# Performance work log

Measured on AMD Instinct MI355X. Metric: run time of the kernel, lower is better.

## Reference

```python
import jax, jax.numpy as jnp
import numpy as np

N_EMBD = 256; N_HEAD = 16; CTX = 2048
V_HD = 32; KV_RANK = 32; Q_RANK = 96
ROPE_HD = 64; NOPE_HD = 32; HEAD_D = ROPE_HD + NOPE_HD  # 96
N_KEEP = CTX // 4  # 512
C_CURV = 1.0
EPS = 1e-6
B, T = 2, 2048


def rmsnorm(x, w):
    return x * jax.lax.rsqrt(jnp.mean(x * x, axis=-1, keepdims=True) + EPS) * w


def logmap(x, u, c):
    # log map from hyperbolic point x toward u (Poincare ball, curvature c)
    xn = jnp.linalg.norm(x, axis=-1, keepdims=True)
    sf = 2.0 / (1.0 + c * xn ** 2)                      # scaling_factor(x, c)
    mx = -x
    un = jnp.linalg.norm(u, axis=-1, keepdims=True)
    ip = jnp.sum(mx * u, axis=-1, keepdims=True)
    num = (1 + 2 * c * ip + c * un ** 2) * mx + (1 - c * xn ** 2) * u
    den = 1 + 2 * c * ip + (c ** 2) * (xn ** 2) * (un ** 2)
    mob = num / den                                      # mobius_addition(-x, u, c)
    an = jnp.linalg.norm(mob, axis=-1, keepdims=True)
    cf = 2.0 / (sf * (c ** 0.5))
    arg = jnp.clip(jnp.sqrt(c) * jnp.sqrt(an), -0.999, 0.999)
    return cf * jnp.arctanh(arg) * (mob / an)


def rope_apply(x, cos_seq, sin_seq):
    # x: [B,H,T,D]; cos/sin: [T,D//2] -> broadcast [1,1,T,D//2]
    c = cos_seq[None, None]; s = sin_seq[None, None]
    xr, xi = jnp.split(x, 2, axis=-1)
    return jnp.concatenate([xr * c - xi * s, xr * s + xi * c], axis=-1)


def attn(q, k, v, causal):
    d = q.shape[-1]
    s = jnp.einsum('bhqd,bhkd->bhqk', q, k) / jnp.sqrt(jnp.asarray(d, q.dtype))
    if causal:
        mask = jnp.tril(jnp.ones((s.shape[-2], s.shape[-1]), bool))
        s = jnp.where(mask, s, -jnp.inf)
    p = jax.nn.softmax(s, axis=-1)
    return jnp.einsum('bhqk,bhkd->bhqd', p, v)


def setup_inputs() -> dict:
    key = jax.random.key(0)
    ks = jax.random.split(key, 20)
    w = lambda k, shp: (jax.random.normal(k, shp, jnp.float32) * 0.02)
    NOPE_DIM = N_HEAD * NOPE_HD   # 512
    ROPE_DIM = N_HEAD * ROPE_HD   # 1024
    VAL_DIM = N_HEAD * V_HD       # 512
    # precompute_freqs_cis(rope_head_dim, ctx_len)
    freqs = 1.0 / (10000.0 ** (np.arange(0, ROPE_HD, 2, dtype=np.float32) / ROPE_HD))
    t = np.arange(CTX, dtype=np.float32)
    ang = np.outer(t, freqs)
    return {
        'x': jax.random.normal(ks[0], (B, T, N_EMBD), jnp.float32),
        'W_cq': w(ks[1], (N_EMBD, Q_RANK)),
        'q_norm_w': jnp.ones((Q_RANK,), jnp.float32),
        'W_dqn': w(ks[2], (Q_RANK, NOPE_DIM)),
        'W_dqr': w(ks[3], (Q_RANK, ROPE_DIM)),
        'W_ckv': w(ks[4], (N_EMBD, KV_RANK)),
        'kv_norm_w': jnp.ones((KV_RANK,), jnp.float32),
        'W_dkn': w(ks[5], (KV_RANK, NOPE_DIM)),
        'W_dv': w(ks[6], (KV_RANK, VAL_DIM)),
        'W_kr': w(ks[7], (N_EMBD, ROPE_HD)),
        'W_imp': w(ks[8], (N_EMBD, 1)),
        'b_imp': jnp.zeros((1,), jnp.float32),
        'W_selk': w(ks[9], (N_EMBD, N_HEAD * HEAD_D)),
        'W_selv': w(ks[10], (N_EMBD, VAL_DIM)),
        'W_wink': w(ks[11], (N_EMBD, N_HEAD * HEAD_D)),
        'W_winv': w(ks[12], (N_EMBD, VAL_DIM)),
        'W_gate': w(ks[13], (N_EMBD, 3)),
        'b_gate': jnp.zeros((3,), jnp.float32),
        'W_proj': w(ks[14], (N_HEAD * V_HD, N_EMBD)),
        'cos_f': jnp.asarray(np.cos(ang)),
        'sin_f': jnp.asarray(np.sin(ang)),
    }


def reference(x, W_cq, q_norm_w, W_dqn, W_dqr, W_ckv, kv_norm_w, W_dkn, W_dv, W_kr,
              W_imp, b_imp, W_selk, W_selv, W_wink, W_winv, W_gate, b_gate, W_proj,
              cos_f, sin_f):
    Bx, Tx, C = x.shape
    ref = jnp.pad(x[:, :-1, :], ((0, 0), (1, 0), (0, 0)))   # calculate_reference_point
    xh = logmap(ref, x, C_CURV)
    # compressed query path
    nq = rmsnorm(xh @ W_cq, q_norm_w)
    qn = (nq @ W_dqn).reshape(Bx, Tx, N_HEAD, NOPE_HD).transpose(0, 2, 1, 3)
    qr = (nq @ W_dqr).reshape(Bx, Tx, N_HEAD, ROPE_HD).transpose(0, 2, 1, 3)
    qr = rope_apply(qr, cos_f[:Tx], sin_f[:Tx])
    q = jnp.concatenate([qn, qr], axis=-1)                  # [B,H,T,96]
    # branch gate
    bw = jax.nn.softmax(jnp.mean(x @ W_gate + b_gate, axis=1), axis=-1)  # [B,3]
    # compressed KV path
    nkv = rmsnorm(x @ W_ckv, kv_norm_w)
    kn = (nkv @ W_dkn).reshape(Bx, Tx, N_HEAD, NOPE_HD).transpose(0, 2, 1, 3)
    v = (nkv @ W_dv).reshape(Bx, Tx, N_HEAD, V_HD).transpose(0, 2, 1, 3)
    kr = rope_apply((x @ W_kr)[:, None], cos_f[:Tx], sin_f[:Tx])  # [B,1,T,64]
    kr = jnp.broadcast_to(kr, (Bx, N_HEAD, Tx, ROPE_HD))
    k = jnp.concatenate([kn, kr], axis=-1)
    out_cmp = attn(q, k, v, causal=True)
    # token-selection branch (top-k important tokens, sorted)
    scores = (x @ W_imp + b_imp)[..., 0]                    # [B,T]
    _, idx = jax.lax.top_k(scores, min(N_KEEP, Tx))
    idx = jnp.sort(idx, axis=1)
    sel = jnp.take_along_axis(x, idx[:, :, None], axis=1)   # [B,K,C]
    sk = (sel @ W_selk).reshape(Bx, -1, N_HEAD, HEAD_D).transpose(0, 2, 1, 3)
    sv = (sel @ W_selv).reshape(Bx, -1, N_HEAD, V_HD).transpose(0, 2, 1, 3)
    out_sel = attn(q, sk, sv, causal=False)
    # sliding-window branch (training path -> full sequence, causal)
    wk = (x @ W_wink).reshape(Bx, Tx, N_HEAD, HEAD_D).transpose(0, 2, 1, 3)
    wv = (x @ W_winv).reshape(Bx, Tx, N_HEAD, V_HD).transpose(0, 2, 1, 3)
    out_win = attn(q, wk, wv, causal=True)
    w3 = bw[:, :, None, None, None]
    out = w3[:, 0] * out_cmp + w3[:, 1] * out_sel + w3[:, 2] * out_win
    out = out.transpose(0, 2, 1, 3).reshape(Bx, Tx, N_HEAD * V_HD)
    return out @ W_proj
```

## Files before the change

kernel.cpp:

```cpp
#include <hip/hip_runtime.h>
#include <hip/hip_bf16.h>
#include <math.h>

#define TT 2048
#define NE 256
#define NHEAD 16

typedef __attribute__((ext_vector_type(8))) short bf16x8;
typedef __attribute__((ext_vector_type(4))) float f32x4;
typedef __attribute__((ext_vector_type(16))) float f32x16;
typedef unsigned short ushort;
typedef __attribute__((ext_vector_type(8))) unsigned short us8;

__device__ __forceinline__ short f2bf(float x) {
  __hip_bfloat16 h = __float2bfloat16(x);
  return *reinterpret_cast<short*>(&h);
}
__device__ __forceinline__ float bf2f(ushort u) {
  unsigned v = ((unsigned)u) << 16;
  return __uint_as_float(v);
}

__global__ __launch_bounds__(256) void prep_kernel(
    const float* __restrict__ x, ushort* __restrict__ xhb, ushort* __restrict__ xbf,
    const float* __restrict__ W_dqn, const float* __restrict__ W_dqr,
    const float* __restrict__ W_dkn, const float* __restrict__ W_dv,
    const float* __restrict__ W_selk, const float* __restrict__ W_selv,
    const float* __restrict__ W_wink, const float* __restrict__ W_winv,
    const float* __restrict__ W_proj, const float* __restrict__ W_cq,
    const float* __restrict__ W_ckv, const float* __restrict__ W_kr,
    const float* __restrict__ W_gate, const float* __restrict__ W_imp,
    ushort* __restrict__ Wt_q, ushort* __restrict__ Wt_kv,
    ushort* __restrict__ Wt_sel, ushort* __restrict__ Wt_win,
    ushort* __restrict__ Wt_proj, ushort* __restrict__ Wt_cq,
    ushort* __restrict__ Wt_nkv, float* __restrict__ gacc) {
  __shared__ float red[16];
  int bx = blockIdx.x, tid = threadIdx.x;
  if (bx < 4096) {
    int row = bx;
    int t = row & (TT - 1);
    float uv = x[row * NE + tid];
    float rv = (t == 0) ? 0.f : x[row * NE - NE + tid];
    xbf[row * NE + tid] = (ushort)f2bf(uv);
    float a = rv * rv, bq = uv * uv, c2 = -rv * uv;
#pragma unroll
    for (int off = 32; off > 0; off >>= 1) {
      a += __shfl_down(a, off, 64);
      bq += __shfl_down(bq, off, 64);
      c2 += __shfl_down(c2, off, 64);
    }
    if ((tid & 63) == 0) {
      int w = tid >> 6;
      red[w] = a; red[4 + w] = bq; red[8 + w] = c2;
    }
    __syncthreads();
    float xn2 = red[0] + red[1] + red[2] + red[3];
    float un2 = red[4] + red[5] + red[6] + red[7];
    float ip  = red[8] + red[9] + red[10] + red[11];
    float den = 1.f + 2.f * ip + xn2 * un2;
    float mob = ((1.f + 2.f * ip + un2) * (-rv) + (1.f - xn2) * uv) / den;
    float m2 = mob * mob;
#pragma unroll
    for (int off = 32; off > 0; off >>= 1) m2 += __shfl_down(m2, off, 64);
    if ((tid & 63) == 0) red[12 + (tid >> 6)] = m2;
    __syncthreads();
    float an2 = red[12] + red[13] + red[14] + red[15];
    float an = sqrtf(an2);
    float cf = 1.f + xn2;
    float arg = fminf(sqrtf(an), 0.999f);
    xhb[row * NE + tid] = (ushort)f2bf(cf * atanhf(arg) * mob / an);
    return;
  }
  int i = (bx - 4096) * 256 + tid;
  const float scale = 0.147244458176154f;
  if (i < 147456) {
    int k = i / 1536, n = i - k * 1536;
    float v = (n < 512) ? W_dqn[(size_t)k * 512 + n] : W_dqr[(size_t)k * 1024 + (n - 512)];
    Wt_q[(size_t)n * 96 + k] = (ushort)f2bf(v * scale);
  } else if (i < 180224) {
    int j = i - 147456;
    int k = j >> 10, n = j & 1023;
    float v = (n < 512) ? W_dkn[(size_t)k * 512 + n] : W_dv[(size_t)k * 512 + (n - 512)];
    Wt_kv[(size_t)n * 32 + k] = (ushort)f2bf(v);
  } else if (i < 704512) {
    int j = i - 180224;
    int k = j >> 11, n = j & 2047;
    float v = (n < 1536) ? W_selk[(size_t)k * 1536 + n] : W_selv[(size_t)k * 512 + (n - 1536)];
    Wt_sel[(size_t)n * 256 + k] = (ushort)f2bf(v);
  } else if (i < 1228800) {
    int j = i - 704512;
    int k = j >> 11, n = j & 2047;
    float v = (n < 1536) ? W_wink[(size_t)k * 1536 + n] : W_winv[(size_t)k * 512 + (n - 1536)];
    Wt_win[(size_t)n * 256 + k] = (ushort)f2bf(v);
  } else if (i < 1359872) {
    int j = i - 1228800;
    int k = j >> 8, n = j & 255;
    Wt_proj[(size_t)n * 512 + k] = (ushort)f2bf(W_proj[(size_t)k * 256 + n]);
  } else if (i < 1392640) {
    int j = i - 1359872;
    int k = j >> 7, n = j & 127;
    float v = (n < 96) ? W_cq[(size_t)k * 96 + n] : 0.f;
    Wt_cq[(size_t)n * 256 + k] = (ushort)f2bf(v);
  } else if (i < 1425408) {
    int j = i - 1392640;
    int k = j >> 7, n = j & 127;
    float v;
    if (n < 32) v = W_ckv[(size_t)k * 32 + n];
    else if (n < 96) v = W_kr[(size_t)k * 64 + (n - 32)];
    else if (n < 99) v = W_gate[(size_t)k * 3 + (n - 96)];
    else if (n == 99) v = W_imp[k];
    else v = 0.f;
    Wt_nkv[(size_t)n * 256 + k] = (ushort)f2bf(v);
  } else if (i < 1425414) {
    gacc[i - 1425408] = 0.f;
  }
}

__global__ __launch_bounds__(256) void gemm_kernel(const ushort* __restrict__ A,
                                                   const ushort* __restrict__ Bt,
                                                   void* __restrict__ Out,
                                                   const ushort* __restrict__ A2,
                                                   const ushort* __restrict__ Bt2,
                                                   void* __restrict__ Out2,
                                                   const int* __restrict__ selidx2,
                                                   const float* __restrict__ cosp,
                                                   const float* __restrict__ sinp,
                                                   float* __restrict__ gateacc,
                                                   int K, int ldo, int obf16, int ropemode,
                                                   int K2, int ldo2, int obf2, int rope2,
                                                   int xlim2, int ylim2) {
  __shared__ __align__(16) short As[128 * 40];
  __shared__ __align__(16) short Bs[128 * 40];
  const int* selidx = nullptr;
  if (blockIdx.z == 1) {
    if ((int)blockIdx.x >= xlim2 || (int)blockIdx.y >= ylim2) return;
    A = A2; Bt = Bt2; Out = Out2; selidx = selidx2;
    K = K2; ldo = ldo2; obf16 = obf2; ropemode = rope2;
  }
  int m0 = blockIdx.x * 128, n0 = blockIdx.y * 128;
  int tid = threadIdx.x;
  int wv = tid >> 6, lane = tid & 63;
  int l15 = lane & 15, quad = lane >> 4;
  int wm = wv >> 1, wn = wv & 1;

  int r = tid >> 1, seg = tid & 1;
  int arow = m0 + r;
  if (selidx) arow = ((arow >> 9) * TT) + selidx[m0 + r];
  const ushort* ga = A + (size_t)arow * K + seg * 16;
  const ushort* gb = Bt + (size_t)(n0 + r) * K + seg * 16;

  f32x4 acc[4][4];
#pragma unroll
  for (int i = 0; i < 4; ++i)
#pragma unroll
    for (int j = 0; j < 4; ++j) acc[i][j] = (f32x4){0.f, 0.f, 0.f, 0.f};

  int nk = K >> 5;
  us8 apre0 = *(const us8*)ga, apre1 = *(const us8*)(ga + 8);
  us8 bpre0 = *(const us8*)gb, bpre1 = *(const us8*)(gb + 8);
  for (int kk = 0; kk < nk; ++kk) {
    __syncthreads();
    *(us8*)(As + r * 40 + seg * 16) = apre0;
    *(us8*)(As + r * 40 + seg * 16 + 8) = apre1;
    *(us8*)(Bs + r * 40 + seg * 16) = bpre0;
    *(us8*)(Bs + r * 40 + seg * 16 + 8) = bpre1;
    __syncthreads();
    if (kk + 1 < nk) {
      apre0 = *(const us8*)(ga + (kk + 1) * 32);
      apre1 = *(const us8*)(ga + (kk + 1) * 32 + 8);
      bpre0 = *(const us8*)(gb + (kk + 1) * 32);
      bpre1 = *(const us8*)(gb + (kk + 1) * 32 + 8);
    }
    bf16x8 af[4], bf[4];
#pragma unroll
    for (int mf = 0; mf < 4; ++mf)
      af[mf] = *(const bf16x8*)(As + (wm * 64 + mf * 16 + l15) * 40 + quad * 8);
#pragma unroll
    for (int nf = 0; nf < 4; ++nf)
      bf[nf] = *(const bf16x8*)(Bs + (wn * 64 + nf * 16 + l15) * 40 + quad * 8);
#pragma unroll
    for (int mf = 0; mf < 4; ++mf)
#pragma unroll
      for (int nf = 0; nf < 4; ++nf)
        acc[mf][nf] = __builtin_amdgcn_mfma_f32_16x16x32_bf16(af[mf], bf[nf], acc[mf][nf], 0, 0, 0);
  }

  if (ropemode && blockIdx.y >= 4) {
#pragma unroll
    for (int mf = 0; mf < 4; ++mf) {
#pragma unroll
      for (int nf = 0; nf < 2; ++nf) {
        int dd = nf * 16 + l15;
#pragma unroll
        for (int reg = 0; reg < 4; ++reg) {
          int row = m0 + wm * 64 + mf * 16 + quad * 4 + reg;
          int t = row & (TT - 1);
          float c = cosp[t * 32 + dd], s = sinp[t * 32 + dd];
          float xr = acc[mf][nf][reg], xi = acc[mf][nf + 2][reg];
          int col = n0 + wn * 64 + nf * 16 + l15;
          size_t oi = (size_t)row * ldo + col;
          ((ushort*)Out)[oi] = (ushort)f2bf(xr * c - xi * s);
          ((ushort*)Out)[oi + 32] = (ushort)f2bf(xr * s + xi * c);
        }
      }
    }
    return;
  }
#pragma unroll
  for (int mf = 0; mf < 4; ++mf) {
#pragma unroll
    for (int nf = 0; nf < 4; ++nf) {
#pragma unroll
      for (int reg = 0; reg < 4; ++reg) {
        int row = m0 + wm * 64 + mf * 16 + quad * 4 + reg;
        int col = n0 + wn * 64 + nf * 16 + l15;
        size_t oi = (size_t)row * ldo + col;
        float v = acc[mf][nf][reg];
        if (obf16) ((ushort*)Out)[oi] = (ushort)f2bf(v);
        else ((float*)Out)[oi] = v;
      }
    }
  }
  if (gateacc != nullptr && blockIdx.z == 1 && wn == 1 && l15 < 3) {
    float ssum = 0.f;
#pragma unroll
    for (int mf = 0; mf < 4; ++mf)
#pragma unroll
      for (int reg = 0; reg < 4; ++reg) ssum += acc[mf][2][reg];
    atomicAdd(&gateacc[(m0 >> 11) * 3 + l15], ssum);
  }
}

__global__ __launch_bounds__(128) void norm_kernel(const float* __restrict__ nkvraw,
                                                   const float* __restrict__ nqraw,
                                                   const float* __restrict__ x,
                                                   const float* __restrict__ W_imp,
                                                   const float* __restrict__ b_imp,
                                                   const float* __restrict__ kvnw,
                                                   const float* __restrict__ qnw,
                                                   const float* __restrict__ cos_t,
                                                   const float* __restrict__ sin_t,
                                                   ushort* __restrict__ nkvb,
                                                   ushort* __restrict__ krbf,
                                                   float* __restrict__ scores,
                                                   ushort* __restrict__ nqb) {
  int tid = threadIdx.x;
  if (blockIdx.x < 4096) {
    int row = blockIdx.x;
    int t = row & (TT - 1);
    if (tid < 32) {
      float v = nkvraw[(size_t)row * 128 + tid];
      float ss = v * v;
#pragma unroll
      for (int off = 16; off > 0; off >>= 1) ss += __shfl_xor(ss, off, 32);
      nkvb[(size_t)row * 32 + tid] = (ushort)f2bf(v * rsqrtf(ss / 32.f + 1e-6f) * kvnw[tid]);
    } else if (tid < 64) {
      int dd = tid - 32;
      float xr = nkvraw[(size_t)row * 128 + 32 + dd];
      float xi = nkvraw[(size_t)row * 128 + 64 + dd];
      float c = cos_t[t * 32 + dd], s = sin_t[t * 32 + dd];
      krbf[(size_t)row * 64 + dd] = (ushort)f2bf(xr * c - xi * s);
      krbf[(size_t)row * 64 + dd + 32] = (ushort)f2bf(xr * s + xi * c);
    } else {
      int lane = tid - 64;
      float p = 0.f;
#pragma unroll
      for (int k = 0; k < 4; ++k) p += x[(size_t)row * 256 + lane + k * 64] * W_imp[lane + k * 64];
#pragma unroll
      for (int off = 32; off > 0; off >>= 1) p += __shfl_down(p, off, 64);
      if (lane == 0) scores[row] = p + b_imp[0];
    }
  } else {
    int row = blockIdx.x - 4096;
    __shared__ float red2[2];
    float v = (tid < 96) ? nqraw[(size_t)row * 128 + tid] : 0.f;
    float p = v * v;
#pragma unroll
    for (int off = 32; off > 0; off >>= 1) p += __shfl_down(p, off, 64);
    if ((tid & 63) == 0) red2[tid >> 6] = p;
    __syncthreads();
    float ss = red2[0] + red2[1];
    float sc = rsqrtf(ss / 96.f + 1e-6f);
    if (tid < 96) nqb[(size_t)row * 96 + tid] = (ushort)f2bf(v * sc * qnw[tid]);
  }
}

__global__ __launch_bounds__(1024) void topk_rank_kernel(const float* __restrict__ scores,
                                                         int* __restrict__ flags) {
  int b = blockIdx.y, blk = blockIdx.x;
  int tid = threadIdx.x;
  __shared__ unsigned sk[TT];
#pragma unroll
  for (int e = 0; e < 2; ++e) {
    int i = tid + e * 1024;
    float s = scores[b * TT + i];
    unsigned u = __float_as_uint(s);
    u = (u & 0x80000000u) ? ~u : (u | 0x80000000u);
    sk[i] = u;
  }
  __syncthreads();
  int e = blk * 64 + (tid >> 4);
  int sub = tid & 15;
  unsigned u = sk[e];
  int r = 0;
  int j0 = sub * 128;
#pragma unroll 8
  for (int j = j0; j < j0 + 128; ++j) {
    unsigned v = sk[j];
    r += (int)((v > u) || (v == u && j < e));
  }
#pragma unroll
  for (int off = 8; off > 0; off >>= 1) r += __shfl_down(r, off, 16);
  if (sub == 0) flags[b * TT + e] = (r < 512) ? 1 : 0;
}

__global__ __launch_bounds__(1024) void topk_scan_kernel(const int* __restrict__ flags,
                                                         int* __restrict__ selidx) {
  int b = blockIdx.x, tid = threadIdx.x;
  __shared__ int wsum[16];
  int2 f = *(const int2*)(flags + b * TT + 2 * tid);
  int local = f.x + f.y;
  int lane = tid & 63, wv = tid >> 6;
  int sc = local;
#pragma unroll
  for (int off = 1; off < 64; off <<= 1) {
    int t = __shfl_up(sc, off, 64);
    if (lane >= off) sc += t;
  }
  if (lane == 63) wsum[wv] = sc;
  __syncthreads();
  int woff = 0;
  for (int w = 0; w < wv; ++w) woff += wsum[w];
  int p0 = woff + (sc - local) + f.x;
  int p1 = p0 + f.y;
  if (f.x) selidx[b * 512 + p0 - 1] = 2 * tid;
  if (f.y) selidx[b * 512 + p1 - 1] = 2 * tid + 1;
}

__global__ __launch_bounds__(512, 4) void flash_fused_kernel(
    const ushort* __restrict__ qbf,
    const ushort* __restrict__ kv,
    const ushort* __restrict__ krbf,
    const ushort* __restrict__ selt,
    const ushort* __restrict__ wint,
    const float* __restrict__ gacc,
    const float* __restrict__ b_gate,
    ushort* __restrict__ attout) {
  __shared__ __align__(16) short smem[13312 + 13312 + 4608 + 256];
  short* Qsm = smem;
  short* Ksm = smem + 13312;
  short* Vtm = smem + 26624;
  float* Ls  = (float*)(smem + 31232);

  int bx = blockIdx.x;
  int j = bx >> 5;
  int qtile = (j < 8) ? (15 - 2 * j) : (2 * (j - 8));
  int bh = bx & 31;
  int b = bh >> 4, h = bh & 15;
  int tid = threadIdx.x;
  int wv = tid >> 6;
  int qsub = wv >> 1;
  int khalf = wv & 1;
  int lane = tid & 63;
  int l31 = lane & 31, half = lane >> 5;

  float w0, w1, w2;
  {
    float g0 = gacc[b * 3 + 0] * (1.0f / 2048.0f) + b_gate[0];
    float g1 = gacc[b * 3 + 1] * (1.0f / 2048.0f) + b_gate[1];
    float g2 = gacc[b * 3 + 2] * (1.0f / 2048.0f) + b_gate[2];
    float mx = fmaxf(g0, fmaxf(g1, g2));
    float e0 = expf(g0 - mx), e1 = expf(g1 - mx), e2 = expf(g2 - mx);
    float inv = 1.f / (e0 + e1 + e2);
    w0 = e0 * inv; w1 = e1 * inv; w2 = e2 * inv;
  }

  int qrow0 = qtile * 128;
  for (int i = tid; i < 128 * 24; i += 512) {
    int qi = i / 24, dp = (i - qi * 24) * 4;
    int col = (dp < 32) ? (h * 32 + dp) : (512 + h * 64 + (dp - 32));
    *(ushort4*)(Qsm + qi * 104 + dp) =
        *(const ushort4*)(qbf + (size_t)(b * TT + qrow0 + qi) * 1536 + col);
  }

  short* kdst[3];
#pragma unroll
  for (int c = 0; c < 3; ++c) {
    int i = c * 512 + tid;
    int kj = i / 24, dp = (i - kj * 24) * 4;
    kdst[c] = &Ksm[kj * 104 + dp];
  }
  int vd0 = (tid & 15) * 2, vkjp = (tid >> 4) * 2;
  short* vdsta = &Vtm[(vd0 + 0) * 72 + vkjp];
  short* vdstb = &Vtm[(vd0 + 1) * 72 + vkjp];

  f32x16 oacc;
#pragma unroll
  for (int r2 = 0; r2 < 16; ++r2) oacc[r2] = 0.f;

#define PREFETCH(KP, VA, VB)                                  \
  {                                                           \
    _Pragma("unroll") for (int c = 0; c < 3; ++c) {           \
      KP[c] = *(const ushort4*)ksrc[c];                       \
      ksrc[c] += kstep[c];                                    \
    }                                                         \
    VA = *(const ushort2*)vsrcA;                              \
    VB = *(const ushort2*)vsrcB;                              \
    vsrcA += vstep;                                           \
    vsrcB += vstep;                                           \
  }

#define COMMIT(KP, VA, VB, SL)                                           \
  {                                                                      \
    _Pragma("unroll") for (int c = 0; c < 3; ++c)                        \
      *(ushort4*)(kdst[c] + (SL) * (64 * 104)) = KP[c];                  \
    *(unsigned*)(vdsta + (SL) * (32 * 72)) =                             \
        (unsigned)VA.x | ((unsigned)VB.x << 16);                         \
    *(unsigned*)(vdstb + (SL) * (32 * 72)) =                             \
        (unsigned)VA.y | ((unsigned)VB.y << 16);                         \
  }

  for (int s = 0; s < 3; ++s) {
    const ushort *kb1, *kb2, *vb;
    size_t krs1, krs2, vrs;
    int split, Tk, causal;
    if (s == 0) {
      kb1 = kv + h * 32;        krs1 = 1024; split = 32;
      kb2 = krbf;               krs2 = 64;
      vb = kv + 512 + h * 32;   vrs = 1024;
      Tk = TT; causal = 1;
    } else if (s == 1) {
      kb1 = selt + h * 96;      krs1 = 2048; split = 96;
      kb2 = selt;               krs2 = 2048;
      vb = selt + 1536 + h * 32; vrs = 2048;
      Tk = 512; causal = 0;
    } else {
      kb1 = wint + h * 96;      krs1 = 2048; split = 96;
      kb2 = wint;               krs2 = 2048;
      vb = wint + 1536 + h * 32; vrs = 2048;
      Tk = TT; causal = 1;
    }
    size_t bTk = (size_t)b * Tk;

    const ushort* ksrc[3];
    int kstep[3];
#pragma unroll
    for (int c = 0; c < 3; ++c) {
      int i = c * 512 + tid;
      int kj = i / 24, dp = (i - kj * 24) * 4;
      if (dp < split) { ksrc[c] = kb1 + (bTk + kj) * krs1 + dp; kstep[c] = (int)(64 * krs1); }
      else            { ksrc[c] = kb2 + (bTk + kj) * krs2 + (dp - split); kstep[c] = (int)(64 * krs2); }
    }
    const ushort* vsrcA = vb + (bTk + vkjp) * vrs + vd0;
    const ushort* vsrcB = vb + (bTk + vkjp + 1) * vrs + vd0;
    int vstep = (int)(64 * vrs);

    ushort4 kpre0[3], kpre1[3];
    ushort2 vpa0, vpb0, vpa1, vpb1;

    f32x16 of;
#pragma unroll
    for (int r2 = 0; r2 < 16; ++r2) of[r2] = 0.f;
    float lsum = 0.f;

    auto do_tile = [&](int kt, const short* Kss, const short* Vss) {
      int krow0 = kt * 64;
      const short* Qrow = Qsm + (qsub * 32 + l31) * 104 + half * 8;
      f32x16 sfT[2];
#pragma unroll
      for (int r2 = 0; r2 < 16; ++r2) { sfT[0][r2] = 0.f; sfT[1][r2] = 0.f; }
#pragma unroll
      for (int ks = 0; ks < 6; ++ks) {
        bf16x8 qk = *(const bf16x8*)(Qrow + ks * 16);
#pragma unroll
        for (int kb = 0; kb < 2; ++kb) {
          bf16x8 ak = *(const bf16x8*)(Kss + (kb * 32 + l31) * 104 + ks * 16 + half * 8);
          sfT[kb] = __builtin_amdgcn_mfma_f32_32x32x16_bf16(ak, qk, sfT[kb], 0, 0, 0);
        }
      }
      int qg = qrow0 + qsub * 32 + l31;
      int domask = causal && (kt >= 2 * qtile);
      unsigned w01[2][4], w23[2][4];
#pragma unroll
      for (int kb = 0; kb < 2; ++kb) {
#pragma unroll
        for (int gg = 0; gg < 4; ++gg) {
          int key0 = krow0 + kb * 32 + 8 * gg + 4 * half;
          float t0 = sfT[kb][gg * 4 + 0];
          float t1 = sfT[kb][gg * 4 + 1];
          float t2 = sfT[kb][gg * 4 + 2];
          float t3 = sfT[kb][gg * 4 + 3];
          if (domask) {
            if (key0 + 0 > qg) t0 = -INFINITY;
            if (key0 + 1 > qg) t1 = -INFINITY;
            if (key0 + 2 > qg) t2 = -INFINITY;
            if (key0 + 3 > qg) t3 = -INFINITY;
          }
          float p0 = __builtin_amdgcn_exp2f(fminf(t0, 43.3f));
          float p1 = __builtin_amdgcn_exp2f(fminf(t1, 43.3f));
          float p2 = __builtin_amdgcn_exp2f(fminf(t2, 43.3f));
          float p3 = __builtin_amdgcn_exp2f(fminf(t3, 43.3f));
          lsum += (p0 + p1) + (p2 + p3);
          asm("v_cvt_pk_bf16_f32 %0, %1, %2" : "=v"(w01[kb][gg]) : "v"(p0), "v"(p1));
          asm("v_cvt_pk_bf16_f32 %0, %1, %2" : "=v"(w23[kb][gg]) : "v"(p2), "v"(p3));
        }
      }
#pragma unroll
      for (int ks2 = 0; ks2 < 4; ++ks2) {
        int kb = ks2 >> 1, gA = 2 * (ks2 & 1);
        unsigned a0 = w01[kb][gA], b0 = w01[kb][gA + 1];
        unsigned a1 = w23[kb][gA], b1 = w23[kb][gA + 1];
        asm("v_permlane32_swap_b32 %0, %1" : "+v"(a0), "+v"(b0));
        asm("v_permlane32_swap_b32 %0, %1" : "+v"(a1), "+v"(b1));
        union { unsigned u[4]; bf16x8 v; } ap;
        ap.u[0] = a0; ap.u[1] = a1; ap.u[2] = b0; ap.u[3] = b1;
        bf16x8 bv = *(const bf16x8*)(Vss + l31 * 72 + ks2 * 16 + half * 8);
        of = __builtin_amdgcn_mfma_f32_32x32x16_bf16(ap.v, bv, of, 0, 0, 0);
      }
    };

    int nkt = causal ? (2 * qtile + 2) : 8;
    PREFETCH(kpre0, vpa0, vpb0);
    PREFETCH(kpre1, vpa1, vpb1);
    for (int kt = 0; kt < nkt; kt += 2) {
      __syncthreads();
      COMMIT(kpre0, vpa0, vpb0, 0);
      COMMIT(kpre1, vpa1, vpb1, 1);
      if (kt + 2 < nkt) PREFETCH(kpre0, vpa0, vpb0);
      if (kt + 3 < nkt) PREFETCH(kpre1, vpa1, vpb1);
      __syncthreads();
      if (khalf == 0) do_tile(kt, Ksm, Vtm);
      else            do_tile(kt + 1, Ksm + 64 * 104, Vtm + 32 * 72);
    }

    lsum += __shfl_xor(lsum, 32, 64);
    __syncthreads();
    float* red = (float*)Ksm;
    int rbase = (qsub * 64 + lane) * 17;
    if (khalf == 1) {
#pragma unroll
      for (int r2 = 0; r2 < 16; ++r2) red[rbase + r2] = of[r2];
      red[rbase + 16] = lsum;
    }
    __syncthreads();
    if (khalf == 0) {
#pragma unroll
      for (int r2 = 0; r2 < 16; ++r2) of[r2] += red[rbase + r2];
      lsum += red[rbase + 16];
      if (half == 0) Ls[qsub * 32 + l31] = lsum;
    }
    asm volatile("s_waitcnt lgkmcnt(0)" ::: "memory");
    if (khalf == 0) {
      float wgt = (s == 0) ? w0 : ((s == 1) ? w1 : w2);
#pragma unroll
      for (int reg = 0; reg < 16; ++reg) {
        int ql = (reg & 3) + 8 * (reg >> 2) + 4 * half;
        oacc[reg] += of[reg] * (wgt / Ls[qsub * 32 + ql]);
      }
    }
  }
#undef PREFETCH
#undef COMMIT

  if (khalf == 0) {
#pragma unroll
    for (int reg = 0; reg < 16; ++reg) {
      int trow = qrow0 + qsub * 32 + (reg & 3) + 8 * (reg >> 2) + 4 * half;
      attout[(size_t)(b * TT + trow) * 512 + h * 32 + l31] = (ushort)f2bf(oacc[reg]);
    }
  }
}

extern "C" void kernel_launch(void* const* d_in, const int* in_sizes, int n_in,
                              void* d_out, int out_size, void* d_ws, size_t ws_size,
                              hipStream_t stream) {
  const float* x      = (const float*)d_in[0];
  const float* W_cq   = (const float*)d_in[1];
  const float* qnw    = (const float*)d_in[2];
  const float* W_dqn  = (const float*)d_in[3];
  const float* W_dqr  = (const float*)d_in[4];
  const float* W_ckv  = (const float*)d_in[5];
  const float* kvnw   = (const float*)d_in[6];
  const float* W_dkn  = (const float*)d_in[7];
  const float* W_dv   = (const float*)d_in[8];
  const float* W_kr   = (const float*)d_in[9];
  const float* W_imp  = (const float*)d_in[10];
  const float* b_imp  = (const float*)d_in[11];
  const float* W_selk = (const float*)d_in[12];
  const float* W_selv = (const float*)d_in[13];
  const float* W_wink = (const float*)d_in[14];
  const float* W_winv = (const float*)d_in[15];
  const float* W_gate = (const float*)d_in[16];
  const float* b_gate = (const float*)d_in[17];
  const float* W_proj = (const float*)d_in[18];
  const float* cos_f  = (const float*)d_in[19];
  const float* sin_f  = (const float*)d_in[20];
  float* out = (float*)d_out;
  float* ws  = (float*)d_ws;

  size_t off = 0;
  auto alloc = [&](size_t n) {
    float* p = ws + off;
    off += (n + 255) & ~(size_t)255;
    return p;
  };
  const int ROWS = 2 * TT;
  ushort* xbf     = (ushort*)alloc((size_t)ROWS * 128);
  ushort* xhb     = (ushort*)alloc((size_t)ROWS * 128);
  float* nqraw    = alloc((size_t)ROWS * 128);
  float* nkvraw   = alloc((size_t)ROWS * 128);
  ushort* nqb     = (ushort*)alloc((size_t)ROWS * 48);
  ushort* qbf     = (ushort*)alloc((size_t)ROWS * 768);
  ushort* nkvb    = (ushort*)alloc((size_t)ROWS * 16);
  ushort* kvtmp   = (ushort*)alloc((size_t)ROWS * 512);
  ushort* krbf    = (ushort*)alloc((size_t)ROWS * 32);
  float* scores   = alloc(ROWS);
  float* gacc     = alloc(8);
  int* selidx     = (int*)alloc(1024);
  int* selflags   = (int*)alloc(ROWS);
  ushort* seltmp  = (ushort*)alloc((size_t)1024 * 1024);
  ushort* wintmp  = (ushort*)alloc((size_t)ROWS * 1024);
  ushort* attoutb = (ushort*)alloc((size_t)ROWS * 256);
  ushort* Wt_q    = (ushort*)alloc((size_t)1536 * 48);
  ushort* Wt_kv   = (ushort*)alloc((size_t)1024 * 16);
  ushort* Wt_sel  = (ushort*)alloc((size_t)2048 * 128);
  ushort* Wt_win  = (ushort*)alloc((size_t)2048 * 128);
  ushort* Wt_proj = (ushort*)alloc((size_t)256 * 256);
  ushort* Wt_cq   = (ushort*)alloc((size_t)128 * 128);
  ushort* Wt_nkv  = (ushort*)alloc((size_t)128 * 128);

  prep_kernel<<<4096 + 5569, 256, 0, stream>>>(
      x, xhb, xbf,
      W_dqn, W_dqr, W_dkn, W_dv, W_selk, W_selv, W_wink, W_winv, W_proj,
      W_cq, W_ckv, W_kr, W_gate, W_imp,
      Wt_q, Wt_kv, Wt_sel, Wt_win, Wt_proj, Wt_cq, Wt_nkv, gacc);

  gemm_kernel<<<dim3(32, 1, 2), 256, 0, stream>>>(
      xhb, Wt_cq, nqraw, xbf, Wt_nkv, nkvraw,
      nullptr, nullptr, nullptr, gacc,
      256, 128, 0, 0, 256, 128, 0, 0, 32, 1);

  norm_kernel<<<2 * ROWS, 128, 0, stream>>>(nkvraw, nqraw, x, W_imp, b_imp, kvnw, qnw,
                                            cos_f, sin_f, nkvb, krbf, scores, nqb);

  gemm_kernel<<<dim3(32, 12, 2), 256, 0, stream>>>(
      nqb, Wt_q, qbf, nkvb, Wt_kv, kvtmp,
      nullptr, cos_f, sin_f, nullptr,
      96, 1536, 1, 1, 32, 1024, 1, 0, 32, 8);

  topk_rank_kernel<<<dim3(32, 2), 1024, 0, stream>>>(scores, selflags);
  topk_scan_kernel<<<2, 1024, 0, stream>>>(selflags, selidx);

  gemm_kernel<<<dim3(32, 16, 2), 256, 0, stream>>>(
      xbf, Wt_win, wintmp, xbf, Wt_sel, seltmp,
      selidx, nullptr, nullptr, nullptr,
      256, 2048, 1, 0, 256, 2048, 1, 0, 8, 16);

  flash_fused_kernel<<<512, 512, 0, stream>>>(qbf, kvtmp, krbf, seltmp, wintmp,
                                              gacc, b_gate, attoutb);

  gemm_kernel<<<dim3(32, 2, 1), 256, 0, stream>>>(
      attoutb, Wt_proj, out, nullptr, nullptr, nullptr,
      nullptr, nullptr, nullptr, nullptr,
      512, 256, 0, 0, 0, 0, 0, 0, 0, 0);
}
```

Baseline: 276.8 us.

## Fuse RMSNorm, key RoPE and importance scores into first GEMM epilogue

Removes the separate norm_kernel by doing the q/kv RMSNorm, the rope on the key-rope projection, the importance score and the gate accumulation inside the epilogue of the first low-rank GEMM. Row sums of squares are reduced with shuffles across the tile and through shared memory, which is reused from the A/B tiles. This avoids writing and rereading the fp32 raw projection buffers and saves one kernel launch. In exchange the GEMM epilogue gains extra syncs and branching, and its stores are scattered.

New measurement: 274.4 us. Within noise of the previous version (-0.8%).

```diff
diff --git a/kernel.cpp b/kernel.cpp
--- a/kernel.cpp
+++ b/kernel.cpp
@@ -126,11 +126,18 @@
                                                    const float* __restrict__ cosp,
                                                    const float* __restrict__ sinp,
                                                    float* __restrict__ gateacc,
+                                                   const float* __restrict__ kvnw,
+                                                   const float* __restrict__ qnw,
+                                                   const float* __restrict__ bimp,
+                                                   ushort* __restrict__ krbf_o,
+                                                   float* __restrict__ scores_o,
+                                                   int fusenorm,
                                                    int K, int ldo, int obf16, int ropemode,
                                                    int K2, int ldo2, int obf2, int rope2,
                                                    int xlim2, int ylim2) {
-  __shared__ __align__(16) short As[128 * 40];
-  __shared__ __align__(16) short Bs[128 * 40];
+  __shared__ __align__(16) short gsm[2 * 128 * 40];
+  short* As = gsm;
+  short* Bs = gsm + 128 * 40;
   const int* selidx = nullptr;
   if (blockIdx.z == 1) {
     if ((int)blockIdx.x >= xlim2 || (int)blockIdx.y >= ylim2) return;
@@ -185,6 +192,119 @@
         acc[mf][nf] = __builtin_amdgcn_mfma_f32_16x16x32_bf16(af[mf], bf[nf], acc[mf][nf], 0, 0, 0);
   }
 
+  if (fusenorm) {
+    __syncthreads();
+    float* sc = (float*)gsm;
+    if (blockIdx.z == 0) {
+      float ss[4][4];
+#pragma unroll
+      for (int mf = 0; mf < 4; ++mf)
+#pragma unroll
+        for (int reg = 0; reg < 4; ++reg) {
+          float p = acc[mf][0][reg] * acc[mf][0][reg] + acc[mf][1][reg] * acc[mf][1][reg];
+          if (wn == 0) p += acc[mf][2][reg] * acc[mf][2][reg] + acc[mf][3][reg] * acc[mf][3][reg];
+#pragma unroll
+          for (int off = 8; off > 0; off >>= 1) p += __shfl_xor(p, off, 64);
+          ss[mf][reg] = p;
+        }
+      if (l15 == 0) {
+#pragma unroll
+        for (int mf = 0; mf < 4; ++mf)
+#pragma unroll
+          for (int reg = 0; reg < 4; ++reg)
+            sc[wn * 128 + wm * 64 + mf * 16 + quad * 4 + reg] = ss[mf][reg];
+      }
+      __syncthreads();
+#pragma unroll
+      for (int mf = 0; mf < 4; ++mf) {
+#pragma unroll
+        for (int nf = 0; nf < 4; ++nf) {
+          if (wn == 1 && nf >= 2) continue;
+          int col = wn * 64 + nf * 16 + l15;
+#pragma unroll
+          for (int reg = 0; reg < 4; ++reg) {
+            int rl = wm * 64 + mf * 16 + quad * 4 + reg;
+            float sstot = sc[rl] + sc[128 + rl];
+            float sca = rsqrtf(sstot / 96.f + 1e-6f) * qnw[col];
+            ((ushort*)Out)[(size_t)(m0 + rl) * 96 + col] = (ushort)f2bf(acc[mf][nf][reg] * sca);
+          }
+        }
+      }
+    } else {
+      if (wn == 1 && l15 < 3) {
+        float g = 0.f;
+#pragma unroll
+        for (int mf = 0; mf < 4; ++mf)
+#pragma unroll
+          for (int reg = 0; reg < 4; ++reg) g += acc[mf][2][reg];
+        atomicAdd(&gateacc[(m0 >> 11) * 3 + l15], g);
+      }
+      if (wn == 1 && l15 == 3) {
+#pragma unroll
+        for (int mf = 0; mf < 4; ++mf)
+#pragma unroll
+          for (int reg = 0; reg < 4; ++reg)
+            scores_o[m0 + wm * 64 + mf * 16 + quad * 4 + reg] = acc[mf][2][reg] + bimp[0];
+      }
+      if (wn == 0) {
+#pragma unroll
+        for (int mf = 0; mf < 4; ++mf) {
+          float ssr[4];
+#pragma unroll
+          for (int reg = 0; reg < 4; ++reg) {
+            float p = acc[mf][0][reg] * acc[mf][0][reg] + acc[mf][1][reg] * acc[mf][1][reg];
+#pragma unroll
+            for (int off = 8; off > 0; off >>= 1) p += __shfl_xor(p, off, 64);
+            ssr[reg] = p;
+          }
+#pragma unroll
+          for (int nf = 0; nf < 2; ++nf) {
+            int col = nf * 16 + l15;
+#pragma unroll
+            for (int reg = 0; reg < 4; ++reg) {
+              int rl = wm * 64 + mf * 16 + quad * 4 + reg;
+              float sca = rsqrtf(ssr[reg] / 32.f + 1e-6f) * kvnw[col];
+              ((ushort*)Out)[(size_t)(m0 + rl) * 32 + col] = (ushort)f2bf(acc[mf][nf][reg] * sca);
+            }
+          }
+        }
+      }
+      if (wn == 1) {
+#pragma unroll
+        for (int mf = 0; mf < 4; ++mf)
+#pragma unroll
+          for (int nf = 0; nf < 2; ++nf) {
+            int dd = nf * 16 + l15;
+#pragma unroll
+            for (int reg = 0; reg < 4; ++reg) {
+              int rl = wm * 64 + mf * 16 + quad * 4 + reg;
+              sc[rl * 33 + dd] = acc[mf][nf][reg];
+            }
+          }
+      }
+      __syncthreads();
+      if (wn == 0) {
+#pragma unroll
+        for (int mf = 0; mf < 4; ++mf)
+#pragma unroll
+          for (int nf = 2; nf < 4; ++nf) {
+            int dd = (nf - 2) * 16 + l15;
+#pragma unroll
+            for (int reg = 0; reg < 4; ++reg) {
+              int rl = wm * 64 + mf * 16 + quad * 4 + reg;
+              int grow = m0 + rl;
+              int t = grow & (TT - 1);
+              float c = cosp[t * 32 + dd], s = sinp[t * 32 + dd];
+              float xr = acc[mf][nf][reg], xi = sc[rl * 33 + dd];
+              krbf_o[(size_t)grow * 64 + dd] = (ushort)f2bf(xr * c - xi * s);
+              krbf_o[(size_t)grow * 64 + dd + 32] = (ushort)f2bf(xr * s + xi * c);
+            }
+          }
+      }
+    }
+    return;
+  }
+
   if (ropemode && blockIdx.y >= 4) {
 #pragma unroll
     for (int mf = 0; mf < 4; ++mf) {
@@ -220,68 +340,6 @@
         else ((float*)Out)[oi] = v;
       }
     }
-  }
-  if (gateacc != nullptr && blockIdx.z == 1 && wn == 1 && l15 < 3) {
-    float ssum = 0.f;
-#pragma unroll
-    for (int mf = 0; mf < 4; ++mf)
-#pragma unroll
-      for (int reg = 0; reg < 4; ++reg) ssum += acc[mf][2][reg];
-    atomicAdd(&gateacc[(m0 >> 11) * 3 + l15], ssum);
-  }
-}
-
-__global__ __launch_bounds__(128) void norm_kernel(const float* __restrict__ nkvraw,
-                                                   const float* __restrict__ nqraw,
-                                                   const float* __restrict__ x,
-                                                   const float* __restrict__ W_imp,
-                                                   const float* __restrict__ b_imp,
-                                                   const float* __restrict__ kvnw,
-                                                   const float* __restrict__ qnw,
-                                                   const float* __restrict__ cos_t,
-                                                   const float* __restrict__ sin_t,
-                                                   ushort* __restrict__ nkvb,
-                                                   ushort* __restrict__ krbf,
-                                                   float* __restrict__ scores,
-                                                   ushort* __restrict__ nqb) {
-  int tid = threadIdx.x;
-  if (blockIdx.x < 4096) {
-    int row = blockIdx.x;
-    int t = row & (TT - 1);
-    if (tid < 32) {
-      float v = nkvraw[(size_t)row * 128 + tid];
-      float ss = v * v;
-#pragma unroll
-      for (int off = 16; off > 0; off >>= 1) ss += __shfl_xor(ss, off, 32);
-      nkvb[(size_t)row * 32 + tid] = (ushort)f2bf(v * rsqrtf(ss / 32.f + 1e-6f) * kvnw[tid]);
-    } else if (tid < 64) {
-      int dd = tid - 32;
-      float xr = nkvraw[(size_t)row * 128 + 32 + dd];
-      float xi = nkvraw[(size_t)row * 128 + 64 + dd];
-      float c = cos_t[t * 32 + dd], s = sin_t[t * 32 + dd];
-      krbf[(size_t)row * 64 + dd] = (ushort)f2bf(xr * c - xi * s);
-      krbf[(size_t)row * 64 + dd + 32] = (ushort)f2bf(xr * s + xi * c);
-    } else {
-      int lane = tid - 64;
-      float p = 0.f;
-#pragma unroll
-      for (int k = 0; k < 4; ++k) p += x[(size_t)row * 256 + lane + k * 64] * W_imp[lane + k * 64];
-#pragma unroll
-      for (int off = 32; off > 0; off >>= 1) p += __shfl_down(p, off, 64);
-      if (lane == 0) scores[row] = p + b_imp[0];
-    }
-  } else {
-    int row = blockIdx.x - 4096;
-    __shared__ float red2[2];
-    float v = (tid < 96) ? nqraw[(size_t)row * 128 + tid] : 0.f;
-    float p = v * v;
-#pragma unroll
-    for (int off = 32; off > 0; off >>= 1) p += __shfl_down(p, off, 64);
-    if ((tid & 63) == 0) red2[tid >> 6] = p;
-    __syncthreads();
-    float ss = red2[0] + red2[1];
-    float sc = rsqrtf(ss / 96.f + 1e-6f);
-    if (tid < 96) nqb[(size_t)row * 96 + tid] = (ushort)f2bf(v * sc * qnw[tid]);
   }
 }
 
@@ -607,8 +665,6 @@
   const int ROWS = 2 * TT;
   ushort* xbf     = (ushort*)alloc((size_t)ROWS * 128);
   ushort* xhb     = (ushort*)alloc((size_t)ROWS * 128);
-  float* nqraw    = alloc((size_t)ROWS * 128);
-  float* nkvraw   = alloc((size_t)ROWS * 128);
   ushort* nqb     = (ushort*)alloc((size_t)ROWS * 48);
   ushort* qbf     = (ushort*)alloc((size_t)ROWS * 768);
   ushort* nkvb    = (ushort*)alloc((size_t)ROWS * 16);
@@ -636,16 +692,15 @@
       Wt_q, Wt_kv, Wt_sel, Wt_win, Wt_proj, Wt_cq, Wt_nkv, gacc);
 
   gemm_kernel<<<dim3(32, 1, 2), 256, 0, stream>>>(
-      xhb, Wt_cq, nqraw, xbf, Wt_nkv, nkvraw,
-      nullptr, nullptr, nullptr, gacc,
-      256, 128, 0, 0, 256, 128, 0, 0, 32, 1);
-
-  norm_kernel<<<2 * ROWS, 128, 0, stream>>>(nkvraw, nqraw, x, W_imp, b_imp, kvnw, qnw,
-                                            cos_f, sin_f, nkvb, krbf, scores, nqb);
+      xhb, Wt_cq, nqb, xbf, Wt_nkv, nkvb,
+      nullptr, cos_f, sin_f, gacc,
+      kvnw, qnw, b_imp, krbf, scores, 1,
+      256, 96, 1, 0, 256, 32, 1, 0, 32, 1);
 
   gemm_kernel<<<dim3(32, 12, 2), 256, 0, stream>>>(
       nqb, Wt_q, qbf, nkvb, Wt_kv, kvtmp,
       nullptr, cos_f, sin_f, nullptr,
+      nullptr, nullptr, nullptr, nullptr, nullptr, 0,
       96, 1536, 1, 1, 32, 1024, 1, 0, 32, 8);
 
   topk_rank_kernel<<<dim3(32, 2), 1024, 0, stream>>>(scores, selflags);
@@ -654,6 +709,7 @@
   gemm_kernel<<<dim3(32, 16, 2), 256, 0, stream>>>(
       xbf, Wt_win, wintmp, xbf, Wt_sel, seltmp,
       selidx, nullptr, nullptr, nullptr,
+      nullptr, nullptr, nullptr, nullptr, nullptr, 0,
       256, 2048, 1, 0, 256, 2048, 1, 0, 8, 16);
 
   flash_fused_kernel<<<512, 512, 0, stream>>>(qbf, kvtmp, krbf, seltmp, wintmp,
@@ -662,5 +718,6 @@
   gemm_kernel<<<dim3(32, 2, 1), 256, 0, stream>>>(
       attoutb, Wt_proj, out, nullptr, nullptr, nullptr,
       nullptr, nullptr, nullptr, nullptr,
+      nullptr, nullptr, nullptr, nullptr, nullptr, 0,
       512, 256, 0, 0, 0, 0, 0, 0, 0, 0);
 }
```
